# Kernel optimization log

Hardware: AMD Instinct MI355X
Metric: run time of the kernel (lower is better)

The kernel has to match this reference:

```python
import jax, jax.numpy as jnp
import numpy as np

T, B, D, A, L = 256, 256, 512, 32, 3
EPS = 1e-6

def _layernorm(x, scale, bias):
    mu = jnp.mean(x, axis=-1, keepdims=True)
    var = jnp.mean(jnp.square(x - mu), axis=-1, keepdims=True)
    return (x - mu) * jax.lax.rsqrt(var + EPS) * scale + bias

def setup_inputs() -> dict:
    key = jax.random.key(0)
    ks = jax.random.split(key, 16)
    def orth(k, shape, scale):
        a = jax.random.normal(k, shape, dtype=jnp.float32)
        q, r = jnp.linalg.qr(a)
        q = q * jnp.sign(jnp.diagonal(r))
        return (scale * q).astype(jnp.float32)
    inp = {
        'hidden': jnp.zeros((B, D), jnp.float32),
        'obs': jax.random.normal(ks[0], (T, B, D), jnp.float32),
        'dones': jax.random.randint(ks[1], (T, B), 0, 2) > 0,
        'avail_actions': jax.random.randint(ks[2], (T, B, A), 0, 2).astype(jnp.int32),
        # MLP stack: 3 Dense(D) + LayerNorm
        'Wm': jnp.stack([orth(jax.random.fold_in(ks[3], l), (D, D), np.sqrt(2)) for l in range(L)]),
        'bm': jnp.zeros((L, D), jnp.float32),
        'lns': jnp.ones((L, D), jnp.float32),
        'lnb': jnp.zeros((L, D), jnp.float32),
        # GRUCell params: input denses ir/iz/in (with bias), hidden denses hr/hz (no bias), hn (bias)
        'Wi': jnp.stack([jax.random.normal(jax.random.fold_in(ks[4], g), (D, D), jnp.float32) / np.sqrt(D) for g in range(3)]),
        'bi': jnp.zeros((3, D), jnp.float32),
        'Wh': jnp.stack([orth(jax.random.fold_in(ks[5], g), (D, D), 1.0) for g in range(3)]),
        'bhn': jnp.zeros((D,), jnp.float32),
        # actor head
        'Wo': orth(ks[6], (D, D), 2.0),
        'bo': jnp.zeros((D,), jnp.float32),
        'ln2s': jnp.ones((D,), jnp.float32),
        'ln2b': jnp.zeros((D,), jnp.float32),
        'Wa': orth(ks[7], (D, A), 0.01),
        'ba': jnp.zeros((A,), jnp.float32),
    }
    return inp

def reference(hidden, obs, dones, avail_actions, Wm, bm, lns, lnb, Wi, bi, Wh, bhn, Wo, bo, ln2s, ln2b, Wa, ba):
    # MLP encoder: Dense -> LayerNorm -> ReLU, x num_layers
    e = obs  # [T,B,D]
    for l in range(Wm.shape[0]):
        e = jax.nn.relu(_layernorm(e @ Wm[l] + bm[l], lns[l], lnb[l]))
    # time-scanned GRU with reset-masked carry (reset -> zeros carry)
    def step(h, xs):
        x, d = xs  # x:[B,D], d:[B]
        h = jnp.where(d[:, None], jnp.zeros_like(h), h)
        r = jax.nn.sigmoid(x @ Wi[0] + bi[0] + h @ Wh[0])
        z = jax.nn.sigmoid(x @ Wi[1] + bi[1] + h @ Wh[1])
        n = jnp.tanh(x @ Wi[2] + bi[2] + r * (h @ Wh[2] + bhn))
        h_new = (1.0 - z) * n + z * h
        return h_new, h_new
    hidden, y = jax.lax.scan(step, hidden, (e, dones))  # y:[T,B,D]
    # actor head
    am = jax.nn.relu(_layernorm(y @ Wo + bo, ln2s, ln2b))
    logits = am @ Wa + ba
    unavail = 1.0 - avail_actions.astype(logits.dtype)
    action_logits = logits - unavail * 1e10
    return hidden, action_logits
```

## Files before the change

### kernel.cpp

```cpp
#include <hip/hip_runtime.h>
#include <hip/hip_bf16.h>
#include <math.h>


#define TTT 256
#define BBB 256
#define DDD 512
#define ACT 32
#define MMM (TTT*BBB)

typedef short bf16x8 __attribute__((ext_vector_type(8)));
typedef float f32x4 __attribute__((ext_vector_type(4)));
typedef unsigned short u16;

__device__ inline u16 f2bf(float f) {
    unsigned int u = __float_as_uint(f);
    u += 0x7fffu + ((u >> 16) & 1u);
    return (u16)(u >> 16);
}
__device__ inline float bf2f(u16 h) { return __uint_as_float(((unsigned int)h) << 16); }

__global__ __launch_bounds__(256) void transpose_cvt_k(
    const float* __restrict__ in, u16* __restrict__ out, int ostride)
{
    __shared__ float tile[32][33];
    const int c = threadIdx.x & 31;
    const int r0 = threadIdx.x >> 5;
    const int bx = blockIdx.x, by = blockIdx.y;
#pragma unroll
    for (int p = 0; p < 4; p++) {
        int r = r0 + p * 8;
        tile[r][c] = in[(size_t)(by * 32 + r) * DDD + bx * 32 + c];
    }
    __syncthreads();
#pragma unroll
    for (int p = 0; p < 4; p++) {
        int r = r0 + p * 8;
        out[(size_t)(bx * 32 + r) * ostride + by * 32 + c] = f2bf(tile[c][r]);
    }
}

template<bool AF32>
__global__ __launch_bounds__(256) void gemm_bf16_k(
    const void* __restrict__ Aptr, const u16* __restrict__ Bt,
    const float* __restrict__ bias, u16* __restrict__ C, int N)
{
    __shared__ u16 As[128 * 64];
    __shared__ u16 Bs[128 * 64];
    const int tid = threadIdx.x;
    const int row0 = blockIdx.x * 128;
    const int col0 = blockIdx.y * 128;
    const int lane = tid & 63, wid = tid >> 6;
    const int wr = wid >> 1, wc = wid & 1;
    const int lm = lane & 15, lq = lane >> 4;

    f32x4 acc[4][4];
#pragma unroll
    for (int i = 0; i < 4; i++)
#pragma unroll
        for (int j = 0; j < 4; j++) acc[i][j] = (f32x4){0.f, 0.f, 0.f, 0.f};

    for (int kc = 0; kc < 8; kc++) {
        const int k0 = kc * 64;
#pragma unroll
        for (int p = 0; p < 4; p++) {
            int g = p * 256 + tid;
            int row = g >> 3, j = g & 7;
            bf16x8 v;
            if (AF32) {
                const float* s = (const float*)Aptr + (size_t)(row0 + row) * DDD + k0 + j * 8;
                float4 a0 = *(const float4*)s;
                float4 a1 = *(const float4*)(s + 4);
                v[0] = (short)f2bf(a0.x); v[1] = (short)f2bf(a0.y);
                v[2] = (short)f2bf(a0.z); v[3] = (short)f2bf(a0.w);
                v[4] = (short)f2bf(a1.x); v[5] = (short)f2bf(a1.y);
                v[6] = (short)f2bf(a1.z); v[7] = (short)f2bf(a1.w);
            } else {
                v = *(const bf16x8*)((const u16*)Aptr + (size_t)(row0 + row) * DDD + k0 + j * 8);
            }
            *(bf16x8*)(As + row * 64 + ((j ^ (row & 7)) << 3)) = v;
        }
#pragma unroll
        for (int p = 0; p < 4; p++) {
            int g = p * 256 + tid;
            int n = g >> 3, j = g & 7;
            bf16x8 v = *(const bf16x8*)(Bt + (size_t)(col0 + n) * DDD + k0 + j * 8);
            *(bf16x8*)(Bs + n * 64 + ((j ^ (n & 7)) << 3)) = v;
        }
        __syncthreads();
#pragma unroll
        for (int ks = 0; ks < 2; ks++) {
            bf16x8 af[4], bfr[4];
#pragma unroll
            for (int i = 0; i < 4; i++) {
                int row = wr * 64 + i * 16 + lm;
                af[i] = *(const bf16x8*)(As + row * 64 + (((ks * 4 + lq) ^ (row & 7)) << 3));
            }
#pragma unroll
            for (int j = 0; j < 4; j++) {
                int n = wc * 64 + j * 16 + lm;
                bfr[j] = *(const bf16x8*)(Bs + n * 64 + (((ks * 4 + lq) ^ (n & 7)) << 3));
            }
#pragma unroll
            for (int i = 0; i < 4; i++)
#pragma unroll
                for (int j = 0; j < 4; j++)
                    acc[i][j] = __builtin_amdgcn_mfma_f32_16x16x32_bf16(af[i], bfr[j], acc[i][j], 0, 0, 0);
        }
        __syncthreads();
    }
#pragma unroll
    for (int j = 0; j < 4; j++) {
        int col = col0 + wc * 64 + j * 16 + lm;
        float bj = bias[col];
#pragma unroll
        for (int i = 0; i < 4; i++) {
            int rb = row0 + wr * 64 + i * 16 + lq * 4;
#pragma unroll
            for (int r = 0; r < 4; r++)
                C[(size_t)(rb + r) * N + col] = f2bf(acc[i][j][r] + bj);
        }
    }
}

__global__ __launch_bounds__(256) void ln_relu_k(
    u16* __restrict__ X, const float* __restrict__ gamma, const float* __restrict__ beta)
{
    const int tid = threadIdx.x;
    const int lane = tid & 63;
    const size_t row = (size_t)blockIdx.x * 4 + (tid >> 6);
    const int c0 = lane * 8;
    u16* px = X + row * DDD + c0;
    bf16x8 v = *(const bf16x8*)px;
    float f[8]; float s = 0.f, s2 = 0.f;
#pragma unroll
    for (int i = 0; i < 8; i++) { f[i] = bf2f((u16)v[i]); s += f[i]; s2 += f[i] * f[i]; }
#pragma unroll
    for (int off = 32; off; off >>= 1) { s += __shfl_xor(s, off); s2 += __shfl_xor(s2, off); }
    float mu = s * (1.f / (float)DDD);
    float rs = rsqrtf(s2 * (1.f / (float)DDD) - mu * mu + 1e-6f);
    float4 g0 = *(const float4*)(gamma + c0), g1 = *(const float4*)(gamma + c0 + 4);
    float4 b0 = *(const float4*)(beta + c0),  b1 = *(const float4*)(beta + c0 + 4);
    float gg[8] = {g0.x, g0.y, g0.z, g0.w, g1.x, g1.y, g1.z, g1.w};
    float bb[8] = {b0.x, b0.y, b0.z, b0.w, b1.x, b1.y, b1.z, b1.w};
    bf16x8 o;
#pragma unroll
    for (int i = 0; i < 8; i++) {
        float yv = (f[i] - mu) * rs * gg[i] + bb[i];
        o[i] = (short)f2bf(fmaxf(yv, 0.f));
    }
    *(bf16x8*)px = o;
}

__global__ __launch_bounds__(256) void logits_k(
    const u16* __restrict__ AM, const float* __restrict__ Wa,
    const float* __restrict__ ba, const int* __restrict__ avail,
    float* __restrict__ out)
{
    __shared__ float xs[8][DDD];
    const int tid = threadIdx.x;
    const size_t row0 = (size_t)blockIdx.x * 8;
    for (int g = tid; g < 8 * 64; g += 256) {
        int r = g >> 6, c8 = (g & 63) * 8;
        bf16x8 v = *(const bf16x8*)(AM + (row0 + r) * DDD + c8);
#pragma unroll
        for (int i = 0; i < 8; i++) xs[r][c8 + i] = bf2f((u16)v[i]);
    }
    __syncthreads();
    const int r = tid >> 5, a = tid & 31;
    float acc = 0.f;
    for (int k = 0; k < DDD; k += 4) {
        float4 xv = *(const float4*)&xs[r][k];
        acc = fmaf(xv.x, Wa[(k + 0) * ACT + a], acc);
        acc = fmaf(xv.y, Wa[(k + 1) * ACT + a], acc);
        acc = fmaf(xv.z, Wa[(k + 2) * ACT + a], acc);
        acc = fmaf(xv.w, Wa[(k + 3) * ACT + a], acc);
    }
    size_t o = (row0 + r) * ACT + a;
    float v = acc + ba[a];
    if (avail[o] == 0) v -= 1e10f;
    out[o] = v;
}

__global__ __launch_bounds__(256) void depth_build_k(
    const int* __restrict__ dones,
    int* __restrict__ keyA, int* __restrict__ pidxA,
    int* __restrict__ counts, int* __restrict__ maxk)
{
    __shared__ int lc[512];
    __shared__ int lmax;
    const int b = threadIdx.x;
    lc[b] = 0; lc[b + 256] = 0;
    if (b == 0) lmax = 0;
    __syncthreads();
    int dprev = 0, mx = 0;
    for (int t = 0; t < TTT; t++) {
        int pos = t * BBB + b;
        int d, pi, k;
        if (dones[pos] != 0)       { d = 0; pi = -1;       k = 0; }
        else if (t == 0)           { d = 0; pi = -2 - b;   k = 1; }
        else                       { d = dprev + 1; pi = pos - BBB; k = d + 1; }
        keyA[pos] = k; pidxA[pos] = pi;
        atomicAdd(&lc[k], 1);
        mx = max(mx, k);
        dprev = d;
    }
    atomicMax(&lmax, mx);
    __syncthreads();
    counts[b] = lc[b];
    counts[b + 256] = lc[b + 256];
    if (b == 0) *maxk = lmax;
}

__global__ void scan_k(const int* __restrict__ counts, int* __restrict__ offs)
{
    if (threadIdx.x == 0) {
        int s = 0;
        for (int i = 0; i < 512; i++) { offs[i] = s; s += counts[i]; }
    }
}

__global__ __launch_bounds__(256) void scatter_k(
    const int* __restrict__ keyA, const int* __restrict__ offs,
    int* __restrict__ cursor, int* __restrict__ list)
{
    __shared__ int lcnt[512];
    __shared__ int lbase[512];
    const int tid = threadIdx.x;
    lcnt[tid] = 0; lcnt[tid + 256] = 0;
    __syncthreads();
    int pos = blockIdx.x * 256 + tid;
    int k = keyA[pos];
    int rank = atomicAdd(&lcnt[k], 1);
    __syncthreads();
    for (int q = tid; q < 512; q += 256) {
        int c = lcnt[q];
        lbase[q] = c ? atomicAdd(&cursor[q], c) : 0;
    }
    __syncthreads();
    list[offs[k] + lbase[k] + rank] = pos;
}

__device__ inline void grid_barrier(int* cnt, int* gen, int nblk)
{
    __syncthreads();
    if (threadIdx.x == 0) {
        __threadfence();
        int g = __hip_atomic_load(gen, __ATOMIC_RELAXED, __HIP_MEMORY_SCOPE_AGENT);
        int a = __hip_atomic_fetch_add(cnt, 1, __ATOMIC_ACQ_REL, __HIP_MEMORY_SCOPE_AGENT);
        if (a == nblk - 1) {
            __hip_atomic_store(cnt, 0, __ATOMIC_RELAXED, __HIP_MEMORY_SCOPE_AGENT);
            __hip_atomic_store(gen, g + 1, __ATOMIC_RELEASE, __HIP_MEMORY_SCOPE_AGENT);
        } else {
            while (__hip_atomic_load(gen, __ATOMIC_RELAXED, __HIP_MEMORY_SCOPE_AGENT) == g)
                __builtin_amdgcn_s_sleep(4);
            (void)__hip_atomic_load(gen, __ATOMIC_ACQUIRE, __HIP_MEMORY_SCOPE_AGENT);
        }
        __threadfence();
    }
    __syncthreads();
}

template<bool YF32>
__global__ __launch_bounds__(256, 2) void gru_depth_k(
    const u16* __restrict__ E, const float* __restrict__ hidden,
    const u16* __restrict__ Wstk, const float* __restrict__ bi,
    const float* __restrict__ bhn,
    const int* __restrict__ list, const int* __restrict__ offs,
    const int* __restrict__ counts, const int* __restrict__ maxk,
    const int* __restrict__ pidxA,
    void* __restrict__ Yv, float* __restrict__ hid_out,
    int* __restrict__ barCnt, int* __restrict__ barGen)
{
    __shared__ u16 As[64 * 256];
    __shared__ int posL[64], pidxL[64];
    __shared__ int sAnyH;
    const int tid = threadIdx.x;
    const int w = tid >> 6, lane = tid & 63;
    const int lm = lane & 15, lq = lane >> 4;
    const int nblk = gridDim.x;
    const int e   = blockIdx.x & 7;
    const int xb  = blockIdx.x >> 3;
    const int nxb = nblk >> 3;

    const int MK = *maxk;
    for (int k = 0; k <= MK; k++) {
        const int nd = counts[k];
        const int off = offs[k];
        const int ntiles = (nd + 63) >> 6;
        const int ntl = (ntiles - e + 7) >> 3;
        const int njl = (ntl > 0) ? (ntl << 2) : 0;
        for (int lj = xb; lj < njl; lj += nxb) {
            const int rt = ((lj >> 2) << 3) + e;
            const int panel = lj & 3;
            bool hasH = false;
            if (tid < 64) {
                int idx = rt * 64 + tid;
                int p = (idx < nd) ? list[off + idx] : -1;
                int pi = (p >= 0) ? pidxA[p] : -1;
                posL[tid] = p;
                pidxL[tid] = pi;
                hasH = (p >= 0) && (pi != -1);
                unsigned long long m = __ballot(hasH);
                if (tid == 0) sAnyH = (m != 0ULL);
            }
            __syncthreads();
            const bool skipH = !sAnyH;

            f32x4 a01[4][4], aX[4][2], aH[4][2];
#pragma unroll
            for (int mt = 0; mt < 4; mt++) {
#pragma unroll
                for (int q = 0; q < 4; q++) a01[mt][q] = (f32x4){0.f, 0.f, 0.f, 0.f};
#pragma unroll
                for (int q = 0; q < 2; q++) {
                    aX[mt][q] = (f32x4){0.f, 0.f, 0.f, 0.f};
                    aH[mt][q] = (f32x4){0.f, 0.f, 0.f, 0.f};
                }
            }

            const int cb = panel * 128 + w * 32;
            const u16* wp[6];
#pragma unroll
            for (int ct = 0; ct < 6; ct++) {
                int gate = ct >> 1;
                int nglob = gate * 512 + cb + ((ct & 1) << 4) + lm;
                wp[ct] = Wstk + (size_t)nglob * 1024 + lq * 8;
            }

            const int nkc = skipH ? 2 : 4;
            for (int kc = 0; kc < nkc; kc++) {
#pragma unroll
                for (int it = 0; it < 8; it++) {
                    int g = it * 256 + tid;
                    int row = g >> 5, jg = g & 31;
                    int kglob = kc * 256 + jg * 8;
                    bf16x8 v = (bf16x8){0, 0, 0, 0, 0, 0, 0, 0};
                    int p = posL[row];
                    if (p >= 0) {
                        if (kglob < 512) {
                            v = *(const bf16x8*)(E + (size_t)p * DDD + kglob);
                        } else {
                            int k2 = kglob - 512;
                            int pi = pidxL[row];
                            if (pi >= 0) {
                                if (YF32) {
                                    const float* s = (const float*)Yv + (size_t)pi * DDD + k2;
                                    float4 a0 = *(const float4*)s;
                                    float4 a1 = *(const float4*)(s + 4);
                                    v[0] = (short)f2bf(a0.x); v[1] = (short)f2bf(a0.y);
                                    v[2] = (short)f2bf(a0.z); v[3] = (short)f2bf(a0.w);
                                    v[4] = (short)f2bf(a1.x); v[5] = (short)f2bf(a1.y);
                                    v[6] = (short)f2bf(a1.z); v[7] = (short)f2bf(a1.w);
                                } else {
                                    v = *(const bf16x8*)((const u16*)Yv + (size_t)pi * DDD + k2);
                                }
                            } else if (pi <= -2) {
                                const float* s = hidden + (size_t)(-pi - 2) * DDD + k2;
                                float4 a0 = *(const float4*)s;
                                float4 a1 = *(const float4*)(s + 4);
                                v[0] = (short)f2bf(a0.x); v[1] = (short)f2bf(a0.y);
                                v[2] = (short)f2bf(a0.z); v[3] = (short)f2bf(a0.w);
                                v[4] = (short)f2bf(a1.x); v[5] = (short)f2bf(a1.y);
                                v[6] = (short)f2bf(a1.z); v[7] = (short)f2bf(a1.w);
                            }
                        }
                    }
                    *(bf16x8*)(As + row * 256 + ((jg ^ (row & 31)) << 3)) = v;
                }
                __syncthreads();

                const bool xpart = (kc < 2);
                const int kgb = kc * 256;
                bf16x8 bfA[6], bfB[6];

#define LOADW(B, KG) \
    _Pragma("unroll") \
    for (int ct = 0; ct < 6; ct++) B[ct] = *(const bf16x8*)(wp[ct] + (KG));

#define COMPW(B, S) \
    _Pragma("unroll") \
    for (int mt = 0; mt < 4; mt++) { \
        int row = mt * 16 + lm; \
        int jgr = (S) * 4 + lq; \
        bf16x8 af = *(const bf16x8*)(As + row * 256 + ((jgr ^ (row & 31)) << 3)); \
        a01[mt][0] = __builtin_amdgcn_mfma_f32_16x16x32_bf16(af, B[0], a01[mt][0], 0, 0, 0); \
        a01[mt][1] = __builtin_amdgcn_mfma_f32_16x16x32_bf16(af, B[1], a01[mt][1], 0, 0, 0); \
        a01[mt][2] = __builtin_amdgcn_mfma_f32_16x16x32_bf16(af, B[2], a01[mt][2], 0, 0, 0); \
        a01[mt][3] = __builtin_amdgcn_mfma_f32_16x16x32_bf16(af, B[3], a01[mt][3], 0, 0, 0); \
        if (xpart) { \
            aX[mt][0] = __builtin_amdgcn_mfma_f32_16x16x32_bf16(af, B[4], aX[mt][0], 0, 0, 0); \
            aX[mt][1] = __builtin_amdgcn_mfma_f32_16x16x32_bf16(af, B[5], aX[mt][1], 0, 0, 0); \
        } else { \
            aH[mt][0] = __builtin_amdgcn_mfma_f32_16x16x32_bf16(af, B[4], aH[mt][0], 0, 0, 0); \
            aH[mt][1] = __builtin_amdgcn_mfma_f32_16x16x32_bf16(af, B[5], aH[mt][1], 0, 0, 0); \
        } \
    }

                LOADW(bfA, kgb + 0 * 32);
#pragma unroll
                for (int sp = 0; sp < 4; sp++) {
                    const int s0 = sp * 2, s1 = sp * 2 + 1;
                    LOADW(bfB, kgb + s1 * 32);
                    COMPW(bfA, s0);
                    if (sp < 3) { LOADW(bfA, kgb + (s1 + 1) * 32); }
                    COMPW(bfB, s1);
                }
#undef LOADW
#undef COMPW
                __syncthreads();
            }

#pragma unroll
            for (int mt = 0; mt < 4; mt++) {
#pragma unroll
                for (int r = 0; r < 4; r++) {
                    int row = mt * 16 + lq * 4 + r;
                    int p = posL[row];
                    if (p < 0) continue;
                    int pi = pidxL[row];
#pragma unroll
                    for (int ct = 0; ct < 2; ct++) {
                        int cglob = cb + ct * 16 + lm;
                        float rpre = a01[mt][ct][r]     + bi[cglob];
                        float zpre = a01[mt][2 + ct][r] + bi[512 + cglob];
                        float xn   = aX[mt][ct][r]      + bi[1024 + cglob];
                        float hn   = aH[mt][ct][r]      + bhn[cglob];
                        float rg = 1.f / (1.f + __expf(-rpre));
                        float zg = 1.f / (1.f + __expf(-zpre));
                        float targ = xn + rg * hn;
                        float t2 = __expf(-2.f * fabsf(targ));
                        float ng = copysignf((1.f - t2) / (1.f + t2), targ);
                        float hp = 0.f;
                        if (pi >= 0)
                            hp = YF32 ? ((const float*)Yv)[(size_t)pi * DDD + cglob]
                                      : bf2f(((const u16*)Yv)[(size_t)pi * DDD + cglob]);
                        else if (pi <= -2)
                            hp = hidden[(size_t)(-pi - 2) * DDD + cglob];
                        float hnew = (1.f - zg) * ng + zg * hp;
                        if (YF32) ((float*)Yv)[(size_t)p * DDD + cglob] = hnew;
                        else      ((u16*)Yv)[(size_t)p * DDD + cglob] = f2bf(hnew);
                    }
                }
            }
            __syncthreads();
        }
        grid_barrier(barCnt, barGen, nblk);
    }

    for (int i = blockIdx.x * 256 + tid; i < BBB * DDD; i += nblk * 256) {
        int b = i >> 9, c = i & 511;
        size_t yi = (size_t)(65280 + b) * DDD + c;
        hid_out[i] = YF32 ? ((const float*)Yv)[yi] : bf2f(((const u16*)Yv)[yi]);
    }
}

extern "C" void kernel_launch(void* const* d_in, const int* in_sizes, int n_in,
                              void* d_out, int out_size, void* d_ws, size_t ws_size,
                              hipStream_t stream)
{
    const float* hidden = (const float*)d_in[0];
    const float* obs    = (const float*)d_in[1];
    const int*   dones  = (const int*)d_in[2];
    const int*   avail  = (const int*)d_in[3];
    const float* Wm     = (const float*)d_in[4];
    const float* bm     = (const float*)d_in[5];
    const float* lns    = (const float*)d_in[6];
    const float* lnb    = (const float*)d_in[7];
    const float* Wi     = (const float*)d_in[8];
    const float* bi     = (const float*)d_in[9];
    const float* Wh     = (const float*)d_in[10];
    const float* bhn    = (const float*)d_in[11];
    const float* Wo     = (const float*)d_in[12];
    const float* bo     = (const float*)d_in[13];
    const float* ln2s   = (const float*)d_in[14];
    const float* ln2b   = (const float*)d_in[15];
    const float* Wa     = (const float*)d_in[16];
    const float* ba     = (const float*)d_in[17];
    float* out = (float*)d_out;

    char* w = (char*)d_ws;
    u16* Wstk = (u16*)w;  w += (size_t)1536 * 1024 * 2;
    u16* WmT  = (u16*)w;  w += (size_t)3 * DDD * DDD * 2;
    u16* WoT  = (u16*)w;  w += (size_t)DDD * DDD * 2;
    int* meta = (int*)w;  w += 8192;
    int* counts = meta;
    int* offs   = meta + 512;
    int* cursor = meta + 1024;
    int* maxk   = meta + 1536;
    int* barCnt = meta + 1568;
    int* barGen = meta + 1600;
    int* keyA   = (int*)w;  w += (size_t)MMM * 4;
    int* pidxA  = (int*)w;  w += (size_t)MMM * 4;
    int* list   = (int*)w;  w += (size_t)MMM * 4;
    u16* P = (u16*)w;       w += (size_t)MMM * DDD * 2;
    void* Yv = (void*)w;
    const size_t base = (size_t)(w - (char*)d_ws);
    const bool yf32 = (ws_size >= base + (size_t)MMM * DDD * 4);

    dim3 tgrid(16, 16);
    for (int l = 0; l < 3; l++)
        transpose_cvt_k<<<tgrid, 256, 0, stream>>>(Wm + (size_t)l * DDD * DDD, WmT + (size_t)l * DDD * DDD, DDD);
    transpose_cvt_k<<<tgrid, 256, 0, stream>>>(Wo, WoT, DDD);
    for (int g = 0; g < 3; g++) {
        transpose_cvt_k<<<tgrid, 256, 0, stream>>>(Wi + (size_t)g * DDD * DDD, Wstk + (size_t)g * 512 * 1024, 1024);
        transpose_cvt_k<<<tgrid, 256, 0, stream>>>(Wh + (size_t)g * DDD * DDD, Wstk + (size_t)g * 512 * 1024 + 512, 1024);
    }
    hipMemsetAsync(meta, 0, 8192, stream);

    depth_build_k<<<1, 256, 0, stream>>>(dones, keyA, pidxA, counts, maxk);
    scan_k<<<1, 64, 0, stream>>>(counts, offs);
    scatter_k<<<MMM / 256, 256, 0, stream>>>(keyA, offs, cursor, list);

    u16* Yq = (u16*)Yv;
    gemm_bf16_k<true><<<dim3(MMM / 128, 4), 256, 0, stream>>>(obs, WmT, bm, P, DDD);
    ln_relu_k<<<dim3(MMM / 4), 256, 0, stream>>>(P, lns, lnb);
    gemm_bf16_k<false><<<dim3(MMM / 128, 4), 256, 0, stream>>>(P, WmT + (size_t)DDD * DDD, bm + DDD, Yq, DDD);
    ln_relu_k<<<dim3(MMM / 4), 256, 0, stream>>>(Yq, lns + DDD, lnb + DDD);
    gemm_bf16_k<false><<<dim3(MMM / 128, 4), 256, 0, stream>>>(Yq, WmT + (size_t)2 * DDD * DDD, bm + 2 * DDD, P, DDD);
    ln_relu_k<<<dim3(MMM / 4), 256, 0, stream>>>(P, lns + 2 * DDD, lnb + 2 * DDD);

    {
        const void* fptr = yf32 ? (const void*)gru_depth_k<true>
                                : (const void*)gru_depth_k<false>;
        int occ = 0;
        hipError_t e = hipOccupancyMaxActiveBlocksPerMultiprocessor(&occ, fptr, 256, 0);
        if (e != hipSuccess || occ < 1) occ = 2;
        if (occ > 4) occ = 4;
        dim3 grid(occ * 256);
        if (yf32)
            gru_depth_k<true><<<grid, 256, 0, stream>>>(
                P, hidden, Wstk, bi, bhn, list, offs, counts, maxk, pidxA,
                Yv, out, barCnt, barGen);
        else
            gru_depth_k<false><<<grid, 256, 0, stream>>>(
                P, hidden, Wstk, bi, bhn, list, offs, counts, maxk, pidxA,
                Yv, out, barCnt, barGen);
    }

    if (yf32)
        gemm_bf16_k<true><<<dim3(MMM / 128, 4), 256, 0, stream>>>(Yv, WoT, bo, P, DDD);
    else
        gemm_bf16_k<false><<<dim3(MMM / 128, 4), 256, 0, stream>>>(Yv, WoT, bo, P, DDD);
    ln_relu_k<<<dim3(MMM / 4), 256, 0, stream>>>(P, ln2s, ln2b);
    logits_k<<<dim3(MMM / 8), 256, 0, stream>>>(P, Wa, ba, avail, out + BBB * DDD);
}
```

Before: 2.181 ms.

## Use two-level per-XCD tree barrier and triple-buffer weight loads in GRU kernel

Replaces the flat grid-wide atomic barrier in the persistent GRU depth kernel with a two-level barrier: blocks first arrive on a per-XCD counter (padded to separate cache lines), then one leader per XCD arrives on a global counter. This is meant to cut contention on a single global atomic at each depth step. The weight-fragment prefetch is also deepened from double to triple buffering so MFMA work can hide more global-load latency. The extra register buffer may raise register pressure and reduce occupancy, and the barrier's correctness relies on blocks mapping to XCDs as blockIdx&7 with nxb blocks per group.

```diff
diff --git a/kernel.cpp b/kernel.cpp
--- a/kernel.cpp
+++ b/kernel.cpp
@@ -241,20 +241,33 @@
     list[offs[k] + lbase[k] + rank] = pos;
 }
 
-__device__ inline void grid_barrier(int* cnt, int* gen, int nblk)
+__device__ inline void tree_barrier(int* xcdCnt, int* xcdGen, int* gCnt, int* gGen,
+                                    int e, int nxb)
 {
     __syncthreads();
     if (threadIdx.x == 0) {
         __threadfence();
-        int g = __hip_atomic_load(gen, __ATOMIC_RELAXED, __HIP_MEMORY_SCOPE_AGENT);
-        int a = __hip_atomic_fetch_add(cnt, 1, __ATOMIC_ACQ_REL, __HIP_MEMORY_SCOPE_AGENT);
-        if (a == nblk - 1) {
-            __hip_atomic_store(cnt, 0, __ATOMIC_RELAXED, __HIP_MEMORY_SCOPE_AGENT);
-            __hip_atomic_store(gen, g + 1, __ATOMIC_RELEASE, __HIP_MEMORY_SCOPE_AGENT);
+        int* xc = xcdCnt + e * 32;
+        int* xg = xcdGen + e * 32;
+        int gx = __hip_atomic_load(xg, __ATOMIC_RELAXED, __HIP_MEMORY_SCOPE_AGENT);
+        int a = __hip_atomic_fetch_add(xc, 1, __ATOMIC_ACQ_REL, __HIP_MEMORY_SCOPE_AGENT);
+        if (a == nxb - 1) {
+            __hip_atomic_store(xc, 0, __ATOMIC_RELAXED, __HIP_MEMORY_SCOPE_AGENT);
+            int gg = __hip_atomic_load(gGen, __ATOMIC_RELAXED, __HIP_MEMORY_SCOPE_AGENT);
+            int b = __hip_atomic_fetch_add(gCnt, 1, __ATOMIC_ACQ_REL, __HIP_MEMORY_SCOPE_AGENT);
+            if (b == 7) {
+                __hip_atomic_store(gCnt, 0, __ATOMIC_RELAXED, __HIP_MEMORY_SCOPE_AGENT);
+                __hip_atomic_store(gGen, gg + 1, __ATOMIC_RELEASE, __HIP_MEMORY_SCOPE_AGENT);
+            } else {
+                while (__hip_atomic_load(gGen, __ATOMIC_RELAXED, __HIP_MEMORY_SCOPE_AGENT) == gg)
+                    __builtin_amdgcn_s_sleep(2);
+                (void)__hip_atomic_load(gGen, __ATOMIC_ACQUIRE, __HIP_MEMORY_SCOPE_AGENT);
+            }
+            __hip_atomic_store(xg, gx + 1, __ATOMIC_RELEASE, __HIP_MEMORY_SCOPE_AGENT);
         } else {
-            while (__hip_atomic_load(gen, __ATOMIC_RELAXED, __HIP_MEMORY_SCOPE_AGENT) == g)
-                __builtin_amdgcn_s_sleep(4);
-            (void)__hip_atomic_load(gen, __ATOMIC_ACQUIRE, __HIP_MEMORY_SCOPE_AGENT);
+            while (__hip_atomic_load(xg, __ATOMIC_RELAXED, __HIP_MEMORY_SCOPE_AGENT) == gx)
+                __builtin_amdgcn_s_sleep(2);
+            (void)__hip_atomic_load(xg, __ATOMIC_ACQUIRE, __HIP_MEMORY_SCOPE_AGENT);
         }
         __threadfence();
     }
@@ -270,7 +283,8 @@
     const int* __restrict__ counts, const int* __restrict__ maxk,
     const int* __restrict__ pidxA,
     void* __restrict__ Yv, float* __restrict__ hid_out,
-    int* __restrict__ barCnt, int* __restrict__ barGen)
+    int* __restrict__ xcdCnt, int* __restrict__ xcdGen,
+    int* __restrict__ gCnt, int* __restrict__ gGen)
 {
     __shared__ u16 As[64 * 256];
     __shared__ int posL[64], pidxL[64];
@@ -372,7 +386,7 @@
 
                 const bool xpart = (kc < 2);
                 const int kgb = kc * 256;
-                bf16x8 bfA[6], bfB[6];
+                bf16x8 bfA[6], bfB[6], bfC[6];
 
 #define LOADW(B, KG) \
     _Pragma("unroll") \
@@ -398,14 +412,16 @@
     }
 
                 LOADW(bfA, kgb + 0 * 32);
-#pragma unroll
-                for (int sp = 0; sp < 4; sp++) {
-                    const int s0 = sp * 2, s1 = sp * 2 + 1;
-                    LOADW(bfB, kgb + s1 * 32);
-                    COMPW(bfA, s0);
-                    if (sp < 3) { LOADW(bfA, kgb + (s1 + 1) * 32); }
-                    COMPW(bfB, s1);
-                }
+                LOADW(bfB, kgb + 1 * 32);
+                LOADW(bfC, kgb + 2 * 32);
+                COMPW(bfA, 0); LOADW(bfA, kgb + 3 * 32);
+                COMPW(bfB, 1); LOADW(bfB, kgb + 4 * 32);
+                COMPW(bfC, 2); LOADW(bfC, kgb + 5 * 32);
+                COMPW(bfA, 3); LOADW(bfA, kgb + 6 * 32);
+                COMPW(bfB, 4); LOADW(bfB, kgb + 7 * 32);
+                COMPW(bfC, 5);
+                COMPW(bfA, 6);
+                COMPW(bfB, 7);
 #undef LOADW
 #undef COMPW
                 __syncthreads();
@@ -445,7 +461,7 @@
             }
             __syncthreads();
         }
-        grid_barrier(barCnt, barGen, nblk);
+        tree_barrier(xcdCnt, xcdGen, gCnt, gGen, e, nxb);
     }
 
     for (int i = blockIdx.x * 256 + tid; i < BBB * DDD; i += nblk * 256) {
@@ -483,13 +499,15 @@
     u16* Wstk = (u16*)w;  w += (size_t)1536 * 1024 * 2;
     u16* WmT  = (u16*)w;  w += (size_t)3 * DDD * DDD * 2;
     u16* WoT  = (u16*)w;  w += (size_t)DDD * DDD * 2;
-    int* meta = (int*)w;  w += 8192;
+    int* meta = (int*)w;  w += 16384;
     int* counts = meta;
     int* offs   = meta + 512;
     int* cursor = meta + 1024;
     int* maxk   = meta + 1536;
-    int* barCnt = meta + 1568;
-    int* barGen = meta + 1600;
+    int* xcdCnt = meta + 1600;
+    int* xcdGen = meta + 1856;
+    int* gCnt   = meta + 2112;
+    int* gGen   = meta + 2144;
     int* keyA   = (int*)w;  w += (size_t)MMM * 4;
     int* pidxA  = (int*)w;  w += (size_t)MMM * 4;
     int* list   = (int*)w;  w += (size_t)MMM * 4;
@@ -506,7 +524,7 @@
         transpose_cvt_k<<<tgrid, 256, 0, stream>>>(Wi + (size_t)g * DDD * DDD, Wstk + (size_t)g * 512 * 1024, 1024);
         transpose_cvt_k<<<tgrid, 256, 0, stream>>>(Wh + (size_t)g * DDD * DDD, Wstk + (size_t)g * 512 * 1024 + 512, 1024);
     }
-    hipMemsetAsync(meta, 0, 8192, stream);
+    hipMemsetAsync(meta, 0, 16384, stream);
 
     depth_build_k<<<1, 256, 0, stream>>>(dones, keyA, pidxA, counts, maxk);
     scan_k<<<1, 64, 0, stream>>>(counts, offs);
@@ -531,11 +549,11 @@
         if (yf32)
             gru_depth_k<true><<<grid, 256, 0, stream>>>(
                 P, hidden, Wstk, bi, bhn, list, offs, counts, maxk, pidxA,
-                Yv, out, barCnt, barGen);
+                Yv, out, xcdCnt, xcdGen, gCnt, gGen);
         else
             gru_depth_k<false><<<grid, 256, 0, stream>>>(
                 P, hidden, Wstk, bi, bhn, list, offs, counts, maxk, pidxA,
-                Yv, out, barCnt, barGen);
+                Yv, out, xcdCnt, xcdGen, gCnt, gGen);
     }
 
     if (yf32)
```

Result: slower. 2.380 ms (+9.1%).

## Use hierarchical XCD barrier and hand sparse depth tail to four blocks

Applied to the files above, without the earlier changes.

Replaces the flat grid-wide barrier between GRU depth levels with a two-level barrier. Blocks first sync within their XCD group, and one representative per group then syncs globally. Depth levels with at most 64 rows, the long sparse tail, are handled by only four blocks with a small 4-block barrier, while the other blocks exit early. This targets the latency of full-grid barriers across many near-empty levels, at the cost of serialising the tail work onto four blocks.

```diff
diff --git a/kernel.cpp b/kernel.cpp
--- a/kernel.cpp
+++ b/kernel.cpp
@@ -19,6 +19,9 @@
     return (u16)(u >> 16);
 }
 __device__ inline float bf2f(u16 h) { return __uint_as_float(((unsigned int)h) << 16); }
+
+#define AL_RLX(p)  __hip_atomic_load((p), __ATOMIC_RELAXED, __HIP_MEMORY_SCOPE_AGENT)
+#define AL_ACQ(p)  __hip_atomic_load((p), __ATOMIC_ACQUIRE, __HIP_MEMORY_SCOPE_AGENT)
 
 __global__ __launch_bounds__(256) void transpose_cvt_k(
     const float* __restrict__ in, u16* __restrict__ out, int ostride)
@@ -212,11 +215,16 @@
     if (b == 0) *maxk = lmax;
 }
 
-__global__ void scan_k(const int* __restrict__ counts, int* __restrict__ offs)
+__global__ void scan_k(const int* __restrict__ counts, int* __restrict__ offs,
+                       int* __restrict__ tailK)
 {
     if (threadIdx.x == 0) {
-        int s = 0;
-        for (int i = 0; i < 512; i++) { offs[i] = s; s += counts[i]; }
+        int s = 0, tk = 0;
+        for (int i = 0; i < 512; i++) {
+            offs[i] = s; s += counts[i];
+            if (counts[i] > 64) tk = i + 1;
+        }
+        *tailK = tk;
     }
 }
 
@@ -241,20 +249,49 @@
     list[offs[k] + lbase[k] + rank] = pos;
 }
 
+__device__ inline void fat_barrier(int* xcdCnt, int* xcdGen, int* gCnt, int* gGen,
+                                   int e, int nxb)
+{
+    __syncthreads();
+    if (threadIdx.x == 0) {
+        int* xc = xcdCnt + e * 32;
+        int* xg = xcdGen + e * 32;
+        int gx = AL_RLX(xg);
+        int a = __hip_atomic_fetch_add(xc, 1, __ATOMIC_RELAXED, __HIP_MEMORY_SCOPE_AGENT);
+        if (a == nxb - 1) {
+            __threadfence();
+            __hip_atomic_store(xc, 0, __ATOMIC_RELAXED, __HIP_MEMORY_SCOPE_AGENT);
+            int gg = AL_RLX(gGen);
+            int b = __hip_atomic_fetch_add(gCnt, 1, __ATOMIC_ACQ_REL, __HIP_MEMORY_SCOPE_AGENT);
+            if (b == 7) {
+                __hip_atomic_store(gCnt, 0, __ATOMIC_RELAXED, __HIP_MEMORY_SCOPE_AGENT);
+                __hip_atomic_store(gGen, gg + 1, __ATOMIC_RELEASE, __HIP_MEMORY_SCOPE_AGENT);
+            } else {
+                while (AL_RLX(gGen) == gg) __builtin_amdgcn_s_sleep(2);
+                (void)AL_ACQ(gGen);
+            }
+            __hip_atomic_store(xg, gx + 1, __ATOMIC_RELEASE, __HIP_MEMORY_SCOPE_AGENT);
+        } else {
+            while (AL_RLX(xg) == gx) __builtin_amdgcn_s_sleep(2);
+            (void)AL_ACQ(xg);
+        }
+    }
+    __syncthreads();
+}
+
 __device__ inline void grid_barrier(int* cnt, int* gen, int nblk)
 {
     __syncthreads();
     if (threadIdx.x == 0) {
         __threadfence();
-        int g = __hip_atomic_load(gen, __ATOMIC_RELAXED, __HIP_MEMORY_SCOPE_AGENT);
+        int g = AL_RLX(gen);
         int a = __hip_atomic_fetch_add(cnt, 1, __ATOMIC_ACQ_REL, __HIP_MEMORY_SCOPE_AGENT);
         if (a == nblk - 1) {
             __hip_atomic_store(cnt, 0, __ATOMIC_RELAXED, __HIP_MEMORY_SCOPE_AGENT);
             __hip_atomic_store(gen, g + 1, __ATOMIC_RELEASE, __HIP_MEMORY_SCOPE_AGENT);
         } else {
-            while (__hip_atomic_load(gen, __ATOMIC_RELAXED, __HIP_MEMORY_SCOPE_AGENT) == g)
-                __builtin_amdgcn_s_sleep(4);
-            (void)__hip_atomic_load(gen, __ATOMIC_ACQUIRE, __HIP_MEMORY_SCOPE_AGENT);
+            while (AL_RLX(gen) == g) __builtin_amdgcn_s_sleep(2);
+            (void)AL_ACQ(gen);
         }
         __threadfence();
     }
@@ -262,117 +299,99 @@
 }
 
 template<bool YF32>
-__global__ __launch_bounds__(256, 2) void gru_depth_k(
+__device__ __forceinline__ void gru_job(
     const u16* __restrict__ E, const float* __restrict__ hidden,
     const u16* __restrict__ Wstk, const float* __restrict__ bi,
     const float* __restrict__ bhn,
-    const int* __restrict__ list, const int* __restrict__ offs,
-    const int* __restrict__ counts, const int* __restrict__ maxk,
-    const int* __restrict__ pidxA,
-    void* __restrict__ Yv, float* __restrict__ hid_out,
-    int* __restrict__ barCnt, int* __restrict__ barGen)
-{
-    __shared__ u16 As[64 * 256];
-    __shared__ int posL[64], pidxL[64];
-    __shared__ int sAnyH;
+    const int* __restrict__ list, const int* __restrict__ pidxA,
+    void* __restrict__ Yv,
+    int off, int nd, int rt, int panel,
+    u16* As, int* posL, int* pidxL, int* sAnyH)
+{
     const int tid = threadIdx.x;
     const int w = tid >> 6, lane = tid & 63;
     const int lm = lane & 15, lq = lane >> 4;
-    const int nblk = gridDim.x;
-    const int e   = blockIdx.x & 7;
-    const int xb  = blockIdx.x >> 3;
-    const int nxb = nblk >> 3;
-
-    const int MK = *maxk;
-    for (int k = 0; k <= MK; k++) {
-        const int nd = counts[k];
-        const int off = offs[k];
-        const int ntiles = (nd + 63) >> 6;
-        const int ntl = (ntiles - e + 7) >> 3;
-        const int njl = (ntl > 0) ? (ntl << 2) : 0;
-        for (int lj = xb; lj < njl; lj += nxb) {
-            const int rt = ((lj >> 2) << 3) + e;
-            const int panel = lj & 3;
-            bool hasH = false;
-            if (tid < 64) {
-                int idx = rt * 64 + tid;
-                int p = (idx < nd) ? list[off + idx] : -1;
-                int pi = (p >= 0) ? pidxA[p] : -1;
-                posL[tid] = p;
-                pidxL[tid] = pi;
-                hasH = (p >= 0) && (pi != -1);
-                unsigned long long m = __ballot(hasH);
-                if (tid == 0) sAnyH = (m != 0ULL);
-            }
-            __syncthreads();
-            const bool skipH = !sAnyH;
-
-            f32x4 a01[4][4], aX[4][2], aH[4][2];
-#pragma unroll
-            for (int mt = 0; mt < 4; mt++) {
-#pragma unroll
-                for (int q = 0; q < 4; q++) a01[mt][q] = (f32x4){0.f, 0.f, 0.f, 0.f};
-#pragma unroll
-                for (int q = 0; q < 2; q++) {
-                    aX[mt][q] = (f32x4){0.f, 0.f, 0.f, 0.f};
-                    aH[mt][q] = (f32x4){0.f, 0.f, 0.f, 0.f};
+
+    bool hasH = false;
+    if (tid < 64) {
+        int idx = rt * 64 + tid;
+        int p = (idx < nd) ? list[off + idx] : -1;
+        int pi = (p >= 0) ? pidxA[p] : -1;
+        posL[tid] = p;
+        pidxL[tid] = pi;
+        hasH = (p >= 0) && (pi != -1);
+        unsigned long long m = __ballot(hasH);
+        if (tid == 0) *sAnyH = (m != 0ULL);
+    }
+    __syncthreads();
+    const bool skipH = !(*sAnyH);
+
+    f32x4 a01[4][4], aX[4][2], aH[4][2];
+#pragma unroll
+    for (int mt = 0; mt < 4; mt++) {
+#pragma unroll
+        for (int q = 0; q < 4; q++) a01[mt][q] = (f32x4){0.f, 0.f, 0.f, 0.f};
+#pragma unroll
+        for (int q = 0; q < 2; q++) {
+            aX[mt][q] = (f32x4){0.f, 0.f, 0.f, 0.f};
+            aH[mt][q] = (f32x4){0.f, 0.f, 0.f, 0.f};
+        }
+    }
+
+    const int cb = panel * 128 + w * 32;
+    const u16* wp[6];
+#pragma unroll
+    for (int ct = 0; ct < 6; ct++) {
+        int gate = ct >> 1;
+        int nglob = gate * 512 + cb + ((ct & 1) << 4) + lm;
+        wp[ct] = Wstk + (size_t)nglob * 1024 + lq * 8;
+    }
+
+    const int nkc = skipH ? 2 : 4;
+    for (int kc = 0; kc < nkc; kc++) {
+#pragma unroll
+        for (int it = 0; it < 8; it++) {
+            int g = it * 256 + tid;
+            int row = g >> 5, jg = g & 31;
+            int kglob = kc * 256 + jg * 8;
+            bf16x8 v = (bf16x8){0, 0, 0, 0, 0, 0, 0, 0};
+            int p = posL[row];
+            if (p >= 0) {
+                if (kglob < 512) {
+                    v = *(const bf16x8*)(E + (size_t)p * DDD + kglob);
+                } else {
+                    int k2 = kglob - 512;
+                    int pi = pidxL[row];
+                    if (pi >= 0) {
+                        if (YF32) {
+                            const float* s = (const float*)Yv + (size_t)pi * DDD + k2;
+                            float4 a0 = *(const float4*)s;
+                            float4 a1 = *(const float4*)(s + 4);
+                            v[0] = (short)f2bf(a0.x); v[1] = (short)f2bf(a0.y);
+                            v[2] = (short)f2bf(a0.z); v[3] = (short)f2bf(a0.w);
+                            v[4] = (short)f2bf(a1.x); v[5] = (short)f2bf(a1.y);
+                            v[6] = (short)f2bf(a1.z); v[7] = (short)f2bf(a1.w);
+                        } else {
+                            v = *(const bf16x8*)((const u16*)Yv + (size_t)pi * DDD + k2);
+                        }
+                    } else if (pi <= -2) {
+                        const float* s = hidden + (size_t)(-pi - 2) * DDD + k2;
+                        float4 a0 = *(const float4*)s;
+                        float4 a1 = *(const float4*)(s + 4);
+                        v[0] = (short)f2bf(a0.x); v[1] = (short)f2bf(a0.y);
+                        v[2] = (short)f2bf(a0.z); v[3] = (short)f2bf(a0.w);
+                        v[4] = (short)f2bf(a1.x); v[5] = (short)f2bf(a1.y);
+                        v[6] = (short)f2bf(a1.z); v[7] = (short)f2bf(a1.w);
+                    }
                 }
             }
-
-            const int cb = panel * 128 + w * 32;
-            const u16* wp[6];
-#pragma unroll
-            for (int ct = 0; ct < 6; ct++) {
-                int gate = ct >> 1;
-                int nglob = gate * 512 + cb + ((ct & 1) << 4) + lm;
-                wp[ct] = Wstk + (size_t)nglob * 1024 + lq * 8;
-            }
-
-            const int nkc = skipH ? 2 : 4;
-            for (int kc = 0; kc < nkc; kc++) {
-#pragma unroll
-                for (int it = 0; it < 8; it++) {
-                    int g = it * 256 + tid;
-                    int row = g >> 5, jg = g & 31;
-                    int kglob = kc * 256 + jg * 8;
-                    bf16x8 v = (bf16x8){0, 0, 0, 0, 0, 0, 0, 0};
-                    int p = posL[row];
-                    if (p >= 0) {
-                        if (kglob < 512) {
-                            v = *(const bf16x8*)(E + (size_t)p * DDD + kglob);
-                        } else {
-                            int k2 = kglob - 512;
-                            int pi = pidxL[row];
-                            if (pi >= 0) {
-                                if (YF32) {
-                                    const float* s = (const float*)Yv + (size_t)pi * DDD + k2;
-                                    float4 a0 = *(const float4*)s;
-                                    float4 a1 = *(const float4*)(s + 4);
-                                    v[0] = (short)f2bf(a0.x); v[1] = (short)f2bf(a0.y);
-                                    v[2] = (short)f2bf(a0.z); v[3] = (short)f2bf(a0.w);
-                                    v[4] = (short)f2bf(a1.x); v[5] = (short)f2bf(a1.y);
-                                    v[6] = (short)f2bf(a1.z); v[7] = (short)f2bf(a1.w);
-                                } else {
-                                    v = *(const bf16x8*)((const u16*)Yv + (size_t)pi * DDD + k2);
-                                }
-                            } else if (pi <= -2) {
-                                const float* s = hidden + (size_t)(-pi - 2) * DDD + k2;
-                                float4 a0 = *(const float4*)s;
-                                float4 a1 = *(const float4*)(s + 4);
-                                v[0] = (short)f2bf(a0.x); v[1] = (short)f2bf(a0.y);
-                                v[2] = (short)f2bf(a0.z); v[3] = (short)f2bf(a0.w);
-                                v[4] = (short)f2bf(a1.x); v[5] = (short)f2bf(a1.y);
-                                v[6] = (short)f2bf(a1.z); v[7] = (short)f2bf(a1.w);
-                            }
-                        }
-                    }
-                    *(bf16x8*)(As + row * 256 + ((jg ^ (row & 31)) << 3)) = v;
-                }
-                __syncthreads();
-
-                const bool xpart = (kc < 2);
-                const int kgb = kc * 256;
-                bf16x8 bfA[6], bfB[6];
+            *(bf16x8*)(As + row * 256 + ((jg ^ (row & 31)) << 3)) = v;
+        }
+        __syncthreads();
+
+        const bool xpart = (kc < 2);
+        const int kgb = kc * 256;
+        bf16x8 bfA[6], bfB[6];
 
 #define LOADW(B, KG) \
     _Pragma("unroll") \
@@ -397,58 +416,108 @@
         } \
     }
 
-                LOADW(bfA, kgb + 0 * 32);
-#pragma unroll
-                for (int sp = 0; sp < 4; sp++) {
-                    const int s0 = sp * 2, s1 = sp * 2 + 1;
-                    LOADW(bfB, kgb + s1 * 32);
-                    COMPW(bfA, s0);
-                    if (sp < 3) { LOADW(bfA, kgb + (s1 + 1) * 32); }
-                    COMPW(bfB, s1);
-                }
+        LOADW(bfA, kgb + 0 * 32);
+#pragma unroll
+        for (int sp = 0; sp < 4; sp++) {
+            const int s0 = sp * 2, s1 = sp * 2 + 1;
+            LOADW(bfB, kgb + s1 * 32);
+            COMPW(bfA, s0);
+            if (sp < 3) { LOADW(bfA, kgb + (s1 + 1) * 32); }
+            COMPW(bfB, s1);
+        }
 #undef LOADW
 #undef COMPW
-                __syncthreads();
+        __syncthreads();
+    }
+
+#pragma unroll
+    for (int mt = 0; mt < 4; mt++) {
+#pragma unroll
+        for (int r = 0; r < 4; r++) {
+            int row = mt * 16 + lq * 4 + r;
+            int p = posL[row];
+            if (p < 0) continue;
+            int pi = pidxL[row];
+#pragma unroll
+            for (int ct = 0; ct < 2; ct++) {
+                int cglob = cb + ct * 16 + lm;
+                float rpre = a01[mt][ct][r]     + bi[cglob];
+                float zpre = a01[mt][2 + ct][r] + bi[512 + cglob];
+                float xn   = aX[mt][ct][r]      + bi[1024 + cglob];
+                float hn   = aH[mt][ct][r]      + bhn[cglob];
+                float rg = 1.f / (1.f + __expf(-rpre));
+                float zg = 1.f / (1.f + __expf(-zpre));
+                float targ = xn + rg * hn;
+                float t2 = __expf(-2.f * fabsf(targ));
+                float ng = copysignf((1.f - t2) / (1.f + t2), targ);
+                float hp = 0.f;
+                if (pi >= 0)
+                    hp = YF32 ? ((const float*)Yv)[(size_t)pi * DDD + cglob]
+                              : bf2f(((const u16*)Yv)[(size_t)pi * DDD + cglob]);
+                else if (pi <= -2)
+                    hp = hidden[(size_t)(-pi - 2) * DDD + cglob];
+                float hnew = (1.f - zg) * ng + zg * hp;
+                if (YF32) ((float*)Yv)[(size_t)p * DDD + cglob] = hnew;
+                else      ((u16*)Yv)[(size_t)p * DDD + cglob] = f2bf(hnew);
             }
-
-#pragma unroll
-            for (int mt = 0; mt < 4; mt++) {
-#pragma unroll
-                for (int r = 0; r < 4; r++) {
-                    int row = mt * 16 + lq * 4 + r;
-                    int p = posL[row];
-                    if (p < 0) continue;
-                    int pi = pidxL[row];
-#pragma unroll
-                    for (int ct = 0; ct < 2; ct++) {
-                        int cglob = cb + ct * 16 + lm;
-                        float rpre = a01[mt][ct][r]     + bi[cglob];
-                        float zpre = a01[mt][2 + ct][r] + bi[512 + cglob];
-                        float xn   = aX[mt][ct][r]      + bi[1024 + cglob];
-                        float hn   = aH[mt][ct][r]      + bhn[cglob];
-                        float rg = 1.f / (1.f + __expf(-rpre));
-                        float zg = 1.f / (1.f + __expf(-zpre));
-                        float targ = xn + rg * hn;
-                        float t2 = __expf(-2.f * fabsf(targ));
-                        float ng = copysignf((1.f - t2) / (1.f + t2), targ);
-                        float hp = 0.f;
-                        if (pi >= 0)
-                            hp = YF32 ? ((const float*)Yv)[(size_t)pi * DDD + cglob]
-                                      : bf2f(((const u16*)Yv)[(size_t)pi * DDD + cglob]);
-                        else if (pi <= -2)
-                            hp = hidden[(size_t)(-pi - 2) * DDD + cglob];
-                        float hnew = (1.f - zg) * ng + zg * hp;
-                        if (YF32) ((float*)Yv)[(size_t)p * DDD + cglob] = hnew;
-                        else      ((u16*)Yv)[(size_t)p * DDD + cglob] = f2bf(hnew);
-                    }
-                }
-            }
-            __syncthreads();
-        }
-        grid_barrier(barCnt, barGen, nblk);
-    }
-
-    for (int i = blockIdx.x * 256 + tid; i < BBB * DDD; i += nblk * 256) {
+        }
+    }
+    __syncthreads();
+}
+
+template<bool YF32>
+__global__ __launch_bounds__(256, 2) void gru_depth_k(
+    const u16* __restrict__ E, const float* __restrict__ hidden,
+    const u16* __restrict__ Wstk, const float* __restrict__ bi,
+    const float* __restrict__ bhn,
+    const int* __restrict__ list, const int* __restrict__ offs,
+    const int* __restrict__ counts, const int* __restrict__ maxk,
+    const int* __restrict__ tailK, const int* __restrict__ pidxA,
+    void* __restrict__ Yv, float* __restrict__ hid_out,
+    int* __restrict__ xcdCnt, int* __restrict__ xcdGen,
+    int* __restrict__ gCnt, int* __restrict__ gGen,
+    int* __restrict__ tCnt, int* __restrict__ tGen)
+{
+    __shared__ u16 As[64 * 256];
+    __shared__ int posL[64], pidxL[64];
+    __shared__ int sAnyH;
+    const int tid = threadIdx.x;
+    const int nblk = gridDim.x;
+    const int e   = blockIdx.x & 7;
+    const int xb  = blockIdx.x >> 3;
+    const int nxb = nblk >> 3;
+
+    const int MK = *maxk;
+    const int TK = *tailK;
+    const int lastFat = (MK < TK - 1) ? MK : (TK - 1);
+
+    for (int k = 0; k <= lastFat; k++) {
+        const int nd = counts[k];
+        const int off = offs[k];
+        const int ntiles = (nd + 63) >> 6;
+        const int ntl = (ntiles - e + 7) >> 3;
+        const int njl = (ntl > 0) ? (ntl << 2) : 0;
+        for (int lj = xb; lj < njl; lj += nxb) {
+            const int rt = ((lj >> 2) << 3) + e;
+            const int panel = lj & 3;
+            gru_job<YF32>(E, hidden, Wstk, bi, bhn, list, pidxA, Yv,
+                          off, nd, rt, panel, As, posL, pidxL, &sAnyH);
+        }
+        fat_barrier(xcdCnt, xcdGen, gCnt, gGen, e, nxb);
+    }
+
+    const bool isTail = (e == 0) && (xb < 4);
+    if (!isTail) return;
+
+    for (int k = TK; k <= MK; k++) {
+        const int nd = counts[k];
+        const int off = offs[k];
+        gru_job<YF32>(E, hidden, Wstk, bi, bhn, list, pidxA, Yv,
+                      off, nd, 0, xb, As, posL, pidxL, &sAnyH);
+        grid_barrier(tCnt, tGen, 4);
+    }
+
+    for (int i = xb * 256 + tid; i < BBB * DDD; i += 1024) {
         int b = i >> 9, c = i & 511;
         size_t yi = (size_t)(65280 + b) * DDD + c;
         hid_out[i] = YF32 ? ((const float*)Yv)[yi] : bf2f(((const u16*)Yv)[yi]);
@@ -483,13 +552,18 @@
     u16* Wstk = (u16*)w;  w += (size_t)1536 * 1024 * 2;
     u16* WmT  = (u16*)w;  w += (size_t)3 * DDD * DDD * 2;
     u16* WoT  = (u16*)w;  w += (size_t)DDD * DDD * 2;
-    int* meta = (int*)w;  w += 8192;
+    int* meta = (int*)w;  w += 16384;
     int* counts = meta;
     int* offs   = meta + 512;
     int* cursor = meta + 1024;
     int* maxk   = meta + 1536;
-    int* barCnt = meta + 1568;
-    int* barGen = meta + 1600;
+    int* tailK  = meta + 1552;
+    int* xcdCnt = meta + 1600;
+    int* xcdGen = meta + 1856;
+    int* gCnt   = meta + 2112;
+    int* gGen   = meta + 2144;
+    int* tCnt   = meta + 2176;
+    int* tGen   = meta + 2208;
     int* keyA   = (int*)w;  w += (size_t)MMM * 4;
     int* pidxA  = (int*)w;  w += (size_t)MMM * 4;
     int* list   = (int*)w;  w += (size_t)MMM * 4;
@@ -506,10 +580,10 @@
         transpose_cvt_k<<<tgrid, 256, 0, stream>>>(Wi + (size_t)g * DDD * DDD, Wstk + (size_t)g * 512 * 1024, 1024);
         transpose_cvt_k<<<tgrid, 256, 0, stream>>>(Wh + (size_t)g * DDD * DDD, Wstk + (size_t)g * 512 * 1024 + 512, 1024);
     }
-    hipMemsetAsync(meta, 0, 8192, stream);
+    hipMemsetAsync(meta, 0, 16384, stream);
 
     depth_build_k<<<1, 256, 0, stream>>>(dones, keyA, pidxA, counts, maxk);
-    scan_k<<<1, 64, 0, stream>>>(counts, offs);
+    scan_k<<<1, 64, 0, stream>>>(counts, offs, tailK);
     scatter_k<<<MMM / 256, 256, 0, stream>>>(keyA, offs, cursor, list);
 
     u16* Yq = (u16*)Yv;
@@ -524,18 +598,18 @@
         const void* fptr = yf32 ? (const void*)gru_depth_k<true>
                                 : (const void*)gru_depth_k<false>;
         int occ = 0;
-        hipError_t e = hipOccupancyMaxActiveBlocksPerMultiprocessor(&occ, fptr, 256, 0);
-        if (e != hipSuccess || occ < 1) occ = 2;
+        hipError_t err = hipOccupancyMaxActiveBlocksPerMultiprocessor(&occ, fptr, 256, 0);
+        if (err != hipSuccess || occ < 1) occ = 2;
         if (occ > 4) occ = 4;
         dim3 grid(occ * 256);
         if (yf32)
             gru_depth_k<true><<<grid, 256, 0, stream>>>(
-                P, hidden, Wstk, bi, bhn, list, offs, counts, maxk, pidxA,
-                Yv, out, barCnt, barGen);
+                P, hidden, Wstk, bi, bhn, list, offs, counts, maxk, tailK, pidxA,
+                Yv, out, xcdCnt, xcdGen, gCnt, gGen, tCnt, tGen);
         else
             gru_depth_k<false><<<grid, 256, 0, stream>>>(
-                P, hidden, Wstk, bi, bhn, list, offs, counts, maxk, pidxA,
-                Yv, out, barCnt, barGen);
+                P, hidden, Wstk, bi, bhn, list, offs, counts, maxk, tailK, pidxA,
+                Yv, out, xcdCnt, xcdGen, gCnt, gGen, tCnt, tGen);
     }
 
     if (yf32)
```

New measurement: 2.006 ms. -8.0%, faster.
